# Optimization experiments

Measured on AMD Instinct MI355X. Metric: run time of the kernel, lower is better.

## Reference

```python
import jax, jax.numpy as jnp
import numpy as np
from jax import lax

KS = 3
R = KS // 2
DILATIONS = (1, 3, 5)


def _fused_ddpm(x, kernels):
    """x: [N,C,H,W]; kernels: [N,3,C,KS*KS,H,W] -> [N,4C,H,W].
    Branch 0 is identity (x); branches 1..3 are per-pixel depthwise conv
    with dilations 1,3,5, zero padding, kernel taken at the output pixel."""
    N, C, H, W = x.shape
    outs = [x]
    for bi, d in enumerate(DILATIONS):
        pad = R * d
        xp = jnp.pad(x, ((0, 0), (0, 0), (pad, pad), (pad, pad)))
        acc = jnp.zeros_like(x)
        for ki in range(KS):
            for kj in range(KS):
                # shifted window: offset (ki-R)*d, (kj-R)*d relative to center
                patch = xp[:, :, ki * d:ki * d + H, kj * d:kj * d + W]
                acc = acc + patch * kernels[:, bi, :, ki * KS + kj]
        outs.append(acc)
    return jnp.concatenate(outs, axis=1)  # [N,4C,H,W]


def setup_inputs() -> dict:
    key = jax.random.key(0)
    k1, k2, k3, k4, k5, k6 = jax.random.split(key, 6)
    N, C, H, W = 4, 64, 128, 128
    x = jax.random.normal(k1, (N, C, H, W), dtype=jnp.float32)
    y = jax.random.normal(k2, (N, C, H, W), dtype=jnp.float32)
    # generator: Conv2d(C, 3*C*KS^2, 1) -> weight [3*C*9, C], bias [3*C*9]
    gen_w = jax.random.normal(k3, (3 * C * KS * KS, C), dtype=jnp.float32) * (1.0 / np.sqrt(C))
    gen_b = jax.random.normal(k4, (3 * C * KS * KS,), dtype=jnp.float32) * 0.01
    # fuse: Conv2d(4C, C, 3, 1, 1) -> weight [C, 4C, 3, 3], bias [C]
    fuse_w = jax.random.normal(k5, (C, 4 * C, 3, 3), dtype=jnp.float32) * (1.0 / np.sqrt(4 * C * 9))
    fuse_b = jax.random.normal(k6, (C,), dtype=jnp.float32) * 0.01
    return {"x": x, "y": y, "gen_w": gen_w, "gen_b": gen_b,
            "fuse_w": fuse_w, "fuse_b": fuse_b}


def reference(x, y, gen_w, gen_b, fuse_w, fuse_b):
    N, C, H, W = x.shape
    # 1x1 conv generator: per-pixel kernels
    k = jnp.einsum('oc,nchw->nohw', gen_w, y) + gen_b[None, :, None, None]
    kernels = k.reshape(N, 3, C, KS * KS, H, W)
    cat_out = _fused_ddpm(x, kernels)  # [N,4C,H,W]
    out = lax.conv_general_dilated(
        cat_out, fuse_w, window_strides=(1, 1), padding=((1, 1), (1, 1)),
        dimension_numbers=('NCHW', 'OIHW', 'NCHW'))
    return out + fuse_b[None, :, None, None]
```

## Files before the change

kernel.cpp:

```cpp
#include <hip/hip_runtime.h>


using f32x4 = __attribute__((ext_vector_type(4))) float;
using u32x4 = __attribute__((ext_vector_type(4))) unsigned;
using s16x8 = __attribute__((ext_vector_type(8))) short;

#define XP_PS 20160

#define OFF_WPK 0u
#define OFF_FW3 55296u
#define OFF_GBP 129024u
#define OFF_XP  131072u
#define OFF_CATP 4325376u

__device__ __forceinline__ unsigned short f2bf(float f) {
    unsigned u = __builtin_bit_cast(unsigned, f);
    u = (u + 0x7fffu + ((u >> 16) & 1u)) >> 16;
    return (unsigned short)u;
}
__device__ __forceinline__ float bflo(unsigned p) {
    return __builtin_bit_cast(float, p << 16);
}
__device__ __forceinline__ float bfhi(unsigned p) {
    return __builtin_bit_cast(float, p & 0xffff0000u);
}

__global__ void k_prep(const float* __restrict__ gen_w,
                       const float* __restrict__ gen_b,
                       const float* __restrict__ fuse_w,
                       const float* __restrict__ x,
                       float* __restrict__ ws) {
    int b = blockIdx.x;
    int t = threadIdx.x;
    if (b < 54) {
        int idx = b * 256 + t;
        if (idx >= 13824) return;
        unsigned short* wpk = (unsigned short*)(ws + OFF_WPK);
        int lane = idx & 63;
        int r = idx >> 6;
        int ks = r & 1; r >>= 1;
        int tile = r % 12, tap = r / 12;
        int comb = tile * 16 + (lane & 15);
        int cc0  = ks * 32 + (lane >> 4) * 8;
        const float* src = gen_w + (size_t)(comb * 9 + tap) * 64 + cc0;
        unsigned short v[8];
#pragma unroll
        for (int j = 0; j < 8; ++j) v[j] = f2bf(src[j]);
        *(s16x8*)(wpk + (size_t)idx * 8) = *(const s16x8*)v;
    } else if (b < 61) {
        int idx = (b - 54) * 256 + t;
        if (idx >= 1728) return;
        int row = idx & 15;
        int r = idx >> 4;
        int tile = r % 12, tap = r / 12;
        ws[OFF_GBP + idx] = gen_b[(tile * 16 + row) * 9 + tap];
    } else if (b < 133) {
        int idx = (b - 61) * 256 + t;
        if (idx >= 18432) return;
        unsigned short* fw3 = (unsigned short*)(ws + OFF_FW3);
        int lane = idx & 63;
        int f = idx >> 6;
        int rt = f & 3; f >>= 2;
        int ks = f & 1; f >>= 1;
        int chunk = f & 3;
        int g = f >> 2;
        int oc = rt * 16 + (lane & 15);
        int ic = chunk * 64 + ks * 32 + (lane >> 4) * 8;
        const float* src = fuse_w + (size_t)oc * 2304 + (size_t)ic * 9 + g;
        unsigned short v[8];
#pragma unroll
        for (int j = 0; j < 8; ++j) v[j] = f2bf(src[j * 9]);
        *(s16x8*)(fw3 + (size_t)idx * 8) = *(const s16x8*)v;
    } else {
        int idx = (b - 133) * 256 + t;
        unsigned* xp = (unsigned*)(ws + OFF_XP);
        int plane = idx / 5040;
        int rem   = idx % 5040;
        int row   = rem / 36;
        int c4    = rem % 36;
        u32x4 v = (u32x4){0u, 0u, 0u, 0u};
        if (row >= 5 && row < 133 && c4 >= 2 && c4 < 34) {
            const float* sx = x + (size_t)(2 * plane) * 16384 +
                              (row - 5) * 128 + (c4 * 4 - 8);
            f32x4 v0 = *(const f32x4*)sx;
            f32x4 v1 = *(const f32x4*)(sx + 16384);
#pragma unroll
            for (int j = 0; j < 4; ++j)
                v[j] = (unsigned)f2bf(v0[j]) | ((unsigned)f2bf(v1[j]) << 16);
        }
        *(u32x4*)(xp + (size_t)plane * XP_PS + row * 144 + c4 * 4) = v;
    }
}

__device__ __forceinline__ void decode_wu(int id, int& h, int& w0, int& n) {
    int wu = (id & 7) * 128 + (id >> 3);
    h = wu & 127;
    int sn = wu >> 7;
    w0 = (sn & 1) << 6;
    n = sn >> 1;
}

__global__ __launch_bounds__(256, 4) void k_gen_mfma(
    const unsigned* __restrict__ xp, const float* __restrict__ y,
    const unsigned short* __restrict__ wpk, const float* __restrict__ gbp,
    unsigned* __restrict__ catp)
{
    __shared__ __align__(16) unsigned Yt[2048];

    int h, w0, n;
    decode_wu(blockIdx.x, h, w0, n);
    const int t = threadIdx.x;
    const int lane = t & 63;
    const int wv = t >> 6;
    const int q = lane >> 4, col = lane & 15;

    {
        const float* yb = y + ((size_t)n * 64) * 16384 + h * 128 + w0 + lane;
#pragma unroll
        for (int p = 0; p < 8; ++p) {
            int cp = wv * 8 + p;
            float a = yb[(size_t)(2 * cp) * 16384];
            float b = yb[(size_t)(2 * cp + 1) * 16384];
            unsigned v = (unsigned)f2bf(a) | ((unsigned)f2bf(b) << 16);
            Yt[(unsigned)(lane * 32 + cp) ^ (((unsigned)(lane & 7)) << 2)] = v;
        }
    }
    __syncthreads();

    s16x8 bfr[4][2];
#pragma unroll
    for (int ctp = 0; ctp < 4; ++ctp)
#pragma unroll
        for (int ks = 0; ks < 2; ++ks) {
            int px = ctp * 16 + col;
            unsigned word = ((unsigned)(px * 32 + ks * 16 + q * 4)) ^
                            (((unsigned)(px & 7)) << 2);
            bfr[ctp][ks] = *(const s16x8*)(Yt + word);
        }

    const int tile0 = wv * 3;
    const unsigned* xn = xp + (size_t)n * 32 * XP_PS;

    float acc[3][4][4];
#pragma unroll
    for (int rt = 0; rt < 3; ++rt)
#pragma unroll
        for (int ctp = 0; ctp < 4; ++ctp)
#pragma unroll
            for (int r = 0; r < 4; ++r) acc[rt][ctp][r] = 0.f;

#pragma unroll 1
    for (int tap = 0; tap < 9; ++tap) {
        const int ti = tap / 3, tj = tap % 3;
        const unsigned short* wp = wpk + ((size_t)(tap * 12 + tile0) * 2 * 64 + lane) * 8;
#pragma unroll
        for (int rt = 0; rt < 3; ++rt) {
            const int tile = tile0 + rt;
            const int bi = tile >> 2;
            const int d  = 2 * bi + 1;
            const int hh = h + (ti - 1) * d;
            const int cb = (tile & 3) * 16 + q * 4;

            f32x4 cinit = *(const f32x4*)(gbp + (size_t)(tap * 12 + tile) * 16 + q * 4);
            s16x8 a0 = *(const s16x8*)(wp + (size_t)(rt * 2 + 0) * 512);
            s16x8 a1 = *(const s16x8*)(wp + (size_t)(rt * 2 + 1) * 512);
#pragma unroll
            for (int ctp = 0; ctp < 4; ++ctp) {
                f32x4 kf = __builtin_amdgcn_mfma_f32_16x16x32_bf16(a0, bfr[ctp][0], cinit, 0, 0, 0);
                kf = __builtin_amdgcn_mfma_f32_16x16x32_bf16(a1, bfr[ctp][1], kf, 0, 0, 0);
                const int ww = w0 + ctp * 16 + col + (tj - 1) * d;
                const unsigned* xr = xn + (size_t)(cb >> 1) * XP_PS +
                                     (hh + 5) * 144 + (ww + 8);
                unsigned p0 = xr[0];
                unsigned p1 = xr[XP_PS];
                acc[rt][ctp][0] = fmaf(kf[0], bflo(p0), acc[rt][ctp][0]);
                acc[rt][ctp][1] = fmaf(kf[1], bfhi(p0), acc[rt][ctp][1]);
                acc[rt][ctp][2] = fmaf(kf[2], bflo(p1), acc[rt][ctp][2]);
                acc[rt][ctp][3] = fmaf(kf[3], bfhi(p1), acc[rt][ctp][3]);
            }
        }
    }

    unsigned* cb0 = catp + (size_t)n * 96 * 16384 + h * 128;
#pragma unroll
    for (int rt = 0; rt < 3; ++rt) {
        const int combr = (tile0 + rt) * 16 + q * 4;
#pragma unroll
        for (int ctp = 0; ctp < 4; ++ctp) {
            const int px = w0 + ctp * 16 + col;
            unsigned v0 = (unsigned)f2bf(acc[rt][ctp][0]) |
                          ((unsigned)f2bf(acc[rt][ctp][1]) << 16);
            unsigned v1 = (unsigned)f2bf(acc[rt][ctp][2]) |
                          ((unsigned)f2bf(acc[rt][ctp][3]) << 16);
            cb0[(size_t)((combr >> 1) + 0) * 16384 + px] = v0;
            cb0[(size_t)((combr >> 1) + 1) * 16384 + px] = v1;
        }
    }
}

__global__ __launch_bounds__(256) void k_fuse_mfma(
    const unsigned* __restrict__ xp, const unsigned* __restrict__ catp,
    const unsigned short* __restrict__ fw3, const float* __restrict__ fuse_b,
    float* __restrict__ out)
{
    __shared__ __align__(16) unsigned Xt[4 * 32 * 68];

    const int id = blockIdx.x;
    const int xcd = id & 7;
    const int unit = id >> 3;
    const int h0 = unit << 1;
    const int n  = xcd >> 1;
    const int w0 = (xcd & 1) << 6;

    const int t = threadIdx.x;
    const int lane = t & 63;
    const int ctp = t >> 6;
    const int col = lane & 15, q = lane >> 4;

    int s_r[8], s_cp[8], s_li[8];
#pragma unroll
    for (int it = 0; it < 8; ++it) {
        int e = it * 256 + t;
        s_r[it]  = e >> 9;
        s_cp[it] = (e >> 4) & 31;
        s_li[it] = e & 15;
    }
    const int hr = t >> 6, hcp = (t >> 1) & 31, hside = t & 1;
    const int hpx = hside ? (w0 + 64) : (w0 - 1);
    const bool hok = ((unsigned)hpx < 128u);

    const int bcol = ctp * 16 + col;
    const int m_kw[3] = { (bcol == 0) ? 64 : bcol - 1,
                          bcol,
                          (bcol == 63) ? 65 : bcol + 1 };

    f32x4 acc[2][4];
#pragma unroll
    for (int row = 0; row < 2; ++row)
#pragma unroll
        for (int rt = 0; rt < 4; ++rt) acc[row][rt] = (f32x4){0.f, 0.f, 0.f, 0.f};

    const unsigned* csrc[4] = {
        nullptr,
        catp + (size_t)n * 96 * 16384,
        catp + ((size_t)n * 96 + 32) * 16384,
        catp + ((size_t)n * 96 + 64) * 16384 };

    auto afp = [&](int chunk, int i) -> const unsigned short* {
        const int g = i >> 1, ks = i & 1;
        return fw3 + ((size_t)((((g * 4 + chunk) * 2 + ks) * 4) * 64 + lane)) * 8;
    };

    u32x4 pf[8];
    unsigned pfh;
    {
        const unsigned* src0 = xp + (size_t)n * 32 * XP_PS;
#pragma unroll
        for (int it = 0; it < 8; ++it)
            pf[it] = *(const u32x4*)(src0 + (size_t)s_cp[it] * XP_PS +
                                     (h0 + 4 + s_r[it]) * 144 + 8 + w0 + s_li[it] * 4);
        pfh = src0[(size_t)hcp * XP_PS + (h0 + 4 + hr) * 144 + 8 + hpx];
    }

#pragma unroll 1
    for (int chunk = 0; chunk < 4; ++chunk) {
        s16x8 afc[4], afn1[4];
        {
            const unsigned short* ap0 = afp(chunk, 0);
            const unsigned short* ap1 = afp(chunk, 1);
#pragma unroll
            for (int rt = 0; rt < 4; ++rt) {
                afc[rt]  = *(const s16x8*)(ap0 + (size_t)rt * 512);
                afn1[rt] = *(const s16x8*)(ap1 + (size_t)rt * 512);
            }
        }

#pragma unroll
        for (int it = 0; it < 8; ++it)
            *(u32x4*)(Xt + (s_r[it] * 32 + s_cp[it]) * 68 + s_li[it] * 4) = pf[it];
        Xt[(hr * 32 + hcp) * 68 + 64 + hside] = pfh;

        __syncthreads();

        if (chunk < 3) {
            const unsigned* src = csrc[chunk + 1];
#pragma unroll
            for (int it = 0; it < 8; ++it) {
                int hh = h0 - 1 + s_r[it];
                u32x4 v = (u32x4){0u, 0u, 0u, 0u};
                if ((unsigned)hh < 128u)
                    v = *(const u32x4*)(src + (size_t)s_cp[it] * 16384 + hh * 128 + w0 + s_li[it] * 4);
                pf[it] = v;
            }
            int hh = h0 - 1 + hr;
            unsigned v = 0u;
            if (hok && (unsigned)hh < 128u)
                v = src[(size_t)hcp * 16384 + hh * 128 + hpx];
            pfh = v;
        }

#pragma unroll
        for (int i = 0; i < 18; ++i) {
            const int g = i >> 1, ks = i & 1;
            const int kh = g / 3, kw = g % 3;

            s16x8 afn2[4];
            if (i < 16) {
                const unsigned short* ap = afp(chunk, i + 2);
#pragma unroll
                for (int rt = 0; rt < 4; ++rt)
                    afn2[rt] = *(const s16x8*)(ap + (size_t)rt * 512);
            }

            const int cpb = ks * 16 + q * 4;
            const int mm = m_kw[kw];
            s16x8 bf[2];
#pragma unroll
            for (int row = 0; row < 2; ++row) {
                const unsigned* bp = Xt + ((row + kh) * 32 + cpb) * 68 + mm;
                unsigned bb[4] = {bp[0], bp[68], bp[136], bp[204]};
                bf[row] = *(const s16x8*)bb;
            }
#pragma unroll
            for (int rt = 0; rt < 4; ++rt)
#pragma unroll
                for (int row = 0; row < 2; ++row)
                    acc[row][rt] = __builtin_amdgcn_mfma_f32_16x16x32_bf16(
                        afc[rt], bf[row], acc[row][rt], 0, 0, 0);

#pragma unroll
            for (int rt = 0; rt < 4; ++rt) {
                afc[rt] = afn1[rt];
                if (i < 16) afn1[rt] = afn2[rt];
            }
        }
        __syncthreads();
    }

    const int px = w0 + ctp * 16 + col;
#pragma unroll
    for (int rt = 0; rt < 4; ++rt) {
        f32x4 fb = *(const f32x4*)(fuse_b + rt * 16 + q * 4);
#pragma unroll
        for (int row = 0; row < 2; ++row)
#pragma unroll
            for (int r = 0; r < 4; ++r) {
                int oc = rt * 16 + q * 4 + r;
                out[((size_t)n * 64 + oc) * 16384 + (h0 + row) * 128 + px] =
                    acc[row][rt][r] + fb[r];
            }
    }
}

extern "C" void kernel_launch(void* const* d_in, const int* in_sizes, int n_in,
                              void* d_out, int out_size, void* d_ws, size_t ws_size,
                              hipStream_t stream) {
    const float* x      = (const float*)d_in[0];
    const float* y      = (const float*)d_in[1];
    const float* gen_w  = (const float*)d_in[2];
    const float* gen_b  = (const float*)d_in[3];
    const float* fuse_w = (const float*)d_in[4];
    const float* fuse_b = (const float*)d_in[5];
    float* out = (float*)d_out;
    float* ws  = (float*)d_ws;

    unsigned* xp   = (unsigned*)(ws + OFF_XP);
    unsigned* catp = (unsigned*)(ws + OFF_CATP);

    k_prep<<<dim3(2653), dim3(256), 0, stream>>>(gen_w, gen_b, fuse_w, x, ws);
    k_gen_mfma<<<dim3(1024), dim3(256), 0, stream>>>(
        xp, y, (const unsigned short*)(ws + OFF_WPK), ws + OFF_GBP, catp);
    k_fuse_mfma<<<dim3(512), dim3(256), 0, stream>>>(
        xp, catp, (const unsigned short*)(ws + OFF_FW3), fuse_b, out);
}
```

Measured before the change: 82.68 us.

## Double-buffer fuse-conv LDS tile and prefetch next chunk's weights across chunks

The fuse MFMA kernel now keeps two LDS buffers for the input tile. Each chunk writes the next chunk's data into the alternate buffer while computing on the current one, and global prefetch runs two chunks ahead. The A-fragment weight pipeline also carries across chunk boundaries, so the first fragments of the next chunk load during the last iterations of the current one. This is meant to remove one barrier per chunk and the load stall at each chunk start, at the cost of doubling LDS use, which may lower occupancy.

```diff
diff --git a/kernel.cpp b/kernel.cpp
--- a/kernel.cpp
+++ b/kernel.cpp
@@ -203,7 +203,7 @@
     const unsigned short* __restrict__ fw3, const float* __restrict__ fuse_b,
     float* __restrict__ out)
 {
-    __shared__ __align__(16) unsigned Xt[4 * 32 * 68];
+    __shared__ __align__(16) unsigned Xt[2][4 * 32 * 68];
 
     const int id = blockIdx.x;
     const int xcd = id & 7;
@@ -261,29 +261,55 @@
                                      (h0 + 4 + s_r[it]) * 144 + 8 + w0 + s_li[it] * 4);
         pfh = src0[(size_t)hcp * XP_PS + (h0 + 4 + hr) * 144 + 8 + hpx];
     }
+    {
+        unsigned* XW = &Xt[0][0];
+#pragma unroll
+        for (int it = 0; it < 8; ++it)
+            *(u32x4*)(XW + (s_r[it] * 32 + s_cp[it]) * 68 + s_li[it] * 4) = pf[it];
+        XW[(hr * 32 + hcp) * 68 + 64 + hside] = pfh;
+    }
+    {
+        const unsigned* src = csrc[1];
+#pragma unroll
+        for (int it = 0; it < 8; ++it) {
+            int hh = h0 - 1 + s_r[it];
+            u32x4 v = (u32x4){0u, 0u, 0u, 0u};
+            if ((unsigned)hh < 128u)
+                v = *(const u32x4*)(src + (size_t)s_cp[it] * 16384 + hh * 128 + w0 + s_li[it] * 4);
+            pf[it] = v;
+        }
+        int hh = h0 - 1 + hr;
+        unsigned v = 0u;
+        if (hok && (unsigned)hh < 128u)
+            v = src[(size_t)hcp * 16384 + hh * 128 + hpx];
+        pfh = v;
+    }
+    s16x8 afc[4], afn1[4];
+    {
+        const unsigned short* ap0 = afp(0, 0);
+        const unsigned short* ap1 = afp(0, 1);
+#pragma unroll
+        for (int rt = 0; rt < 4; ++rt) {
+            afc[rt]  = *(const s16x8*)(ap0 + (size_t)rt * 512);
+            afn1[rt] = *(const s16x8*)(ap1 + (size_t)rt * 512);
+        }
+    }
+    __syncthreads();
 
 #pragma unroll 1
     for (int chunk = 0; chunk < 4; ++chunk) {
-        s16x8 afc[4], afn1[4];
-        {
-            const unsigned short* ap0 = afp(chunk, 0);
-            const unsigned short* ap1 = afp(chunk, 1);
-#pragma unroll
-            for (int rt = 0; rt < 4; ++rt) {
-                afc[rt]  = *(const s16x8*)(ap0 + (size_t)rt * 512);
-                afn1[rt] = *(const s16x8*)(ap1 + (size_t)rt * 512);
-            }
-        }
-
-#pragma unroll
-        for (int it = 0; it < 8; ++it)
-            *(u32x4*)(Xt + (s_r[it] * 32 + s_cp[it]) * 68 + s_li[it] * 4) = pf[it];
-        Xt[(hr * 32 + hcp) * 68 + 64 + hside] = pfh;
-
-        __syncthreads();
+        const unsigned* XB = &Xt[chunk & 1][0];
 
         if (chunk < 3) {
-            const unsigned* src = csrc[chunk + 1];
+            unsigned* XW = &Xt[(chunk + 1) & 1][0];
+#pragma unroll
+            for (int it = 0; it < 8; ++it)
+                *(u32x4*)(XW + (s_r[it] * 32 + s_cp[it]) * 68 + s_li[it] * 4) = pf[it];
+            XW[(hr * 32 + hcp) * 68 + 64 + hside] = pfh;
+        }
+
+        if (chunk < 2) {
+            const unsigned* src = csrc[chunk + 2];
 #pragma unroll
             for (int it = 0; it < 8; ++it) {
                 int hh = h0 - 1 + s_r[it];
@@ -305,8 +331,10 @@
             const int kh = g / 3, kw = g % 3;
 
             s16x8 afn2[4];
-            if (i < 16) {
-                const unsigned short* ap = afp(chunk, i + 2);
+            const bool ld2 = (i < 16) || (chunk < 3);
+            if (ld2) {
+                const unsigned short* ap = (i < 16) ? afp(chunk, i + 2)
+                                                    : afp(chunk + 1, i - 16);
 #pragma unroll
                 for (int rt = 0; rt < 4; ++rt)
                     afn2[rt] = *(const s16x8*)(ap + (size_t)rt * 512);
@@ -317,7 +345,7 @@
             s16x8 bf[2];
 #pragma unroll
             for (int row = 0; row < 2; ++row) {
-                const unsigned* bp = Xt + ((row + kh) * 32 + cpb) * 68 + mm;
+                const unsigned* bp = XB + ((row + kh) * 32 + cpb) * 68 + mm;
                 unsigned bb[4] = {bp[0], bp[68], bp[136], bp[204]};
                 bf[row] = *(const s16x8*)bb;
             }
@@ -331,7 +359,7 @@
 #pragma unroll
             for (int rt = 0; rt < 4; ++rt) {
                 afc[rt] = afn1[rt];
-                if (i < 16) afn1[rt] = afn2[rt];
+                if (ld2) afn1[rt] = afn2[rt];
             }
         }
         __syncthreads();
```

Measured after the change: 79.04 us. -4.4%, faster.
